# Performance work log

Measured on AMD Instinct MI355X. Metric: run time of the kernel, lower is better.

Reference implementation:

```python
import jax, jax.numpy as jnp
import numpy as np

E, H, D = 400000, 8, 64  # edges, num_head, dim_dh
N, G = 40000, 10000      # nodes, generated nodes
PRO = 30000              # pro_nodes_num


def setup_inputs() -> dict:
    key = jax.random.key(0)
    ks = jax.random.split(key, 12)
    a_ij = jax.random.normal(ks[0], (E, H, D), dtype=jnp.float32)
    pos = jax.random.normal(ks[1], (N, 3), dtype=jnp.float32)
    generate_node_dist = jax.random.uniform(ks[2], (G,), dtype=jnp.float32)
    edge_index = jax.random.randint(ks[3], (2, E), 0, N, dtype=jnp.int64)
    parent_node_idxes = jax.random.randint(ks[4], (G,), 0, N, dtype=jnp.int64)
    generate_node_idxes = jax.random.randint(ks[5], (G,), 0, N, dtype=jnp.int64)
    mask_edge_inv = jax.random.randint(ks[6], (E, 1), 0, 2, dtype=jnp.int32).astype(jnp.bool_)
    # MLP params: Linear(D, D//2) -> LeakyReLU -> Linear(D//2, 1); head mixer Linear(H, 1, bias=False)
    W1 = jax.random.normal(ks[7], (D, D // 2), dtype=jnp.float32) / np.sqrt(D)
    b1 = jnp.zeros((D // 2,), dtype=jnp.float32)
    W2 = jax.random.normal(ks[8], (D // 2,), dtype=jnp.float32) / np.sqrt(D // 2)
    b2 = jnp.zeros((1,), dtype=jnp.float32)
    Wh = jax.random.normal(ks[9], (H,), dtype=jnp.float32) / np.sqrt(H)
    return {
        "a_ij": a_ij, "pos": pos, "generate_node_dist": generate_node_dist,
        "edge_index": edge_index, "parent_node_idxes": parent_node_idxes,
        "generate_node_idxes": generate_node_idxes, "mask_edge_inv": mask_edge_inv,
        "pro_nodes_num": PRO,
        "W1": W1, "b1": b1, "W2": W2, "b2": b2, "Wh": Wh,
    }


def reference(a_ij, pos, generate_node_dist, edge_index, parent_node_idxes,
              generate_node_idxes, mask_edge_inv, pro_nodes_num,
              W1, b1, W2, b2, Wh):
    src, dst = edge_index[0], edge_index[1]  # [E]
    # Original filters edges where src >= pro_nodes_num; we keep static shapes and
    # zero the contribution of filtered edges instead (identical scatter-sum result).
    edge_keep = src >= pro_nodes_num                       # [E]
    valid = edge_keep & (~mask_edge_inv[:, 0])             # [E]

    delta_x = pos[src] - pos[dst]                          # [E,3]
    norm = jnp.linalg.norm(delta_x, axis=-1, keepdims=True)
    delta_x = delta_x / (norm + 1e-6)
    delta_x = jnp.where(valid[:, None], delta_x, 0.0)      # mask_edge_inv + dropped edges

    # attention2deltax MLP (dropout inactive at inference): [E,H,D] -> [E,H]
    h = jax.nn.leaky_relu(jnp.einsum('ehd,df->ehf', a_ij, W1) + b1)
    s = jnp.einsum('ehf,f->eh', h, W2) + b2                # [E,H]
    attention = jnp.einsum('eh,h->e', s, Wh)               # weighted_head_layer, [E]

    delta_x = delta_x * attention[:, None]                 # [E,3]
    agg = jax.ops.segment_sum(delta_x, src, num_segments=pos.shape[0])  # [N,3]
    return pos[generate_node_idxes] + agg[generate_node_idxes]
```

## Files before the change

kernel.cpp:

```cpp
#include <hip/hip_runtime.h>

typedef short s8v __attribute__((ext_vector_type(8)));
typedef float f4v __attribute__((ext_vector_type(4)));
typedef unsigned short u16;
typedef unsigned int   u32;
typedef unsigned long long u64;

#define NHEAD 8
#define FDIM  32

__device__ __forceinline__ u16 f2bf(float f) {
    u32 u = __float_as_uint(f);
    u32 r = u + 0x7fffu + ((u >> 16) & 1u);
    return (u16)(r >> 16);
}

__device__ __forceinline__ void detect_ints(const void* maskp, const void* eidxp,
                                            int lane, int& mbyte, int& i64f) {
    u32 mkw = ((const u32*)maskp)[lane];
    mbyte = (__ballot(mkw > 1u) != 0ull) ? 1 : 0;
    u32 od = ((const u32*)eidxp)[2 * lane + 1];
    i64f = (__ballot(od != 0u) == 0ull) ? 1 : 0;
}

struct WaveCtx {
    s8v bfrag[2][2];
    float sumWh, b2v, b1c0, b1c1, w2c0, w2c1;
    float wh0, wh1, wh2, wh3;
};

__device__ __forceinline__ WaveCtx setup_wave(int lane,
    const void* W1p, const void* b1p, const void* W2p, const void* b2p, const void* Whp)
{
    WaveCtx w;
    const int c0 = lane & 15;
    const int krow = (lane >> 4) * 8;
    const int hi4  = (lane >> 4) & 1;
    const float* w1 = (const float*)W1p; const float* b1 = (const float*)b1p;
    const float* w2 = (const float*)W2p; const float* b2 = (const float*)b2p;
    const float* wh = (const float*)Whp;
    float WhV[NHEAD]; w.sumWh = 0.f;
    #pragma unroll
    for (int h = 0; h < NHEAD; ++h) { WhV[h] = wh[h]; w.sumWh += WhV[h]; }
    w.b2v = b2[0];
    w.b1c0 = b1[c0]; w.b1c1 = b1[c0 + 16];
    w.w2c0 = w2[c0]; w.w2c1 = w2[c0 + 16];
    #pragma unroll
    for (int cb = 0; cb < 2; ++cb)
        #pragma unroll
        for (int kh = 0; kh < 2; ++kh)
            #pragma unroll
            for (int j = 0; j < 8; ++j) {
                int k = kh * 32 + krow + j;
                w.bfrag[cb][kh][j] = (short)f2bf(w1[k * FDIM + cb * 16 + c0]);
            }
    w.wh0 = hi4 ? WhV[4] : WhV[0];
    w.wh1 = hi4 ? WhV[5] : WhV[1];
    w.wh2 = hi4 ? WhV[6] : WhV[2];
    w.wh3 = hi4 ? WhV[7] : WhV[3];
    return w;
}

__device__ __forceinline__ void load_tile(const float* a32, int edge, int row, int krow,
                                          s8v& a0, s8v& a1)
{
    const size_t rowbase = ((size_t)edge * 8 + (size_t)(row & 7)) * 64 + (size_t)krow;
    const f4v* p = (const f4v*)(a32 + rowbase);
    f4v v0 = p[0], v1 = p[1], v2 = p[8], v3 = p[9];
    #pragma unroll
    for (int j = 0; j < 4; ++j) {
        a0[j]     = (short)f2bf(v0[j]);
        a0[j + 4] = (short)f2bf(v1[j]);
        a1[j]     = (short)f2bf(v2[j]);
        a1[j + 4] = (short)f2bf(v3[j]);
    }
}

__device__ __forceinline__ float tile_att(const WaveCtx& w, const s8v& a0, const s8v& a1)
{
    f4v C0 = {0.f,0.f,0.f,0.f}, C1 = {0.f,0.f,0.f,0.f};
    C0 = __builtin_amdgcn_mfma_f32_16x16x32_bf16(a0, w.bfrag[0][0], C0, 0, 0, 0);
    C0 = __builtin_amdgcn_mfma_f32_16x16x32_bf16(a1, w.bfrag[0][1], C0, 0, 0, 0);
    C1 = __builtin_amdgcn_mfma_f32_16x16x32_bf16(a0, w.bfrag[1][0], C1, 0, 0, 0);
    C1 = __builtin_amdgcn_mfma_f32_16x16x32_bf16(a1, w.bfrag[1][1], C1, 0, 0, 0);

    float partial;
    {
        float x0, x1, trow;
        x0 = C0[0] + w.b1c0; x0 = (x0 >= 0.f) ? x0 : 0.01f * x0;
        x1 = C1[0] + w.b1c1; x1 = (x1 >= 0.f) ? x1 : 0.01f * x1;
        trow = x0 * w.w2c0 + x1 * w.w2c1; partial  = trow * w.wh0;
        x0 = C0[1] + w.b1c0; x0 = (x0 >= 0.f) ? x0 : 0.01f * x0;
        x1 = C1[1] + w.b1c1; x1 = (x1 >= 0.f) ? x1 : 0.01f * x1;
        trow = x0 * w.w2c0 + x1 * w.w2c1; partial += trow * w.wh1;
        x0 = C0[2] + w.b1c0; x0 = (x0 >= 0.f) ? x0 : 0.01f * x0;
        x1 = C1[2] + w.b1c1; x1 = (x1 >= 0.f) ? x1 : 0.01f * x1;
        trow = x0 * w.w2c0 + x1 * w.w2c1; partial += trow * w.wh2;
        x0 = C0[3] + w.b1c0; x0 = (x0 >= 0.f) ? x0 : 0.01f * x0;
        x1 = C1[3] + w.b1c1; x1 = (x1 >= 0.f) ? x1 : 0.01f * x1;
        trow = x0 * w.w2c0 + x1 * w.w2c1; partial += trow * w.wh3;
    }
    partial += __shfl_xor(partial, 1);
    partial += __shfl_xor(partial, 2);
    partial += __shfl_xor(partial, 4);
    partial += __shfl_xor(partial, 8);
    partial += __shfl_xor(partial, 16);
    return partial + w.b2v * w.sumWh;
}

__global__ __launch_bounds__(256)
void zero_kernel(float* __restrict__ agg, u32* __restrict__ ind, int N3, int N)
{
    int i = blockIdx.x * blockDim.x + threadIdx.x;
    if (i < N3) agg[i] = 0.f;
    if (i < N)  ind[i] = 0u;
}

__global__ __launch_bounds__(256)
void mark_kernel(const void* __restrict__ gidxp, u32* __restrict__ ind,
                 const void* __restrict__ maskp, const void* __restrict__ eidxp, int G)
{
    const int lane = threadIdx.x & 63;
    int mbyte, i64f;
    detect_ints(maskp, eidxp, lane, mbyte, i64f);
    (void)mbyte;
    int g = blockIdx.x * blockDim.x + threadIdx.x;
    if (g >= G) return;
    const int idx = i64f ? (int)((const long long*)gidxp)[g] : ((const int*)gidxp)[g];
    ind[idx] = 1u;
}

__global__ __launch_bounds__(256, 4)
void attn_kernel(const void* __restrict__ a_ij,
                 const void* __restrict__ pos,
                 const void* __restrict__ eidx,
                 const void* __restrict__ maskp,
                 const int*  __restrict__ proP,
                 const void* __restrict__ W1p,
                 const void* __restrict__ b1p,
                 const void* __restrict__ W2p,
                 const void* __restrict__ b2p,
                 const void* __restrict__ Whp,
                 float* __restrict__ agg,
                 const u32* __restrict__ ind,
                 int E)
{
    __shared__ float attbuf[4][68];
    __shared__ int   idxbuf[4][68];

    const int lane = threadIdx.x & 63;
    const int wv   = threadIdx.x >> 6;
    const int gw = blockIdx.x * 4 + wv;
    const int nchunks = (E + 63) >> 6;
    if (gw >= nchunks) return;

    const int base = gw << 6;
    const int ie = base + lane;

    const int*   e32 = (const int*)eidx;
    const long long* e64 = (const long long*)eidx;
    const unsigned char* m8 = (const unsigned char*)maskp;
    const int*   m32 = (const int*)maskp;

    int s32 = 0; long long s64 = 0; int m8v = 1;
    if (ie < E) { s32 = e32[ie]; s64 = e64[ie]; m8v = (int)m8[ie]; }
    const int pro = proP[0];

    int mbyte, i64f;
    detect_ints(maskp, eidx, lane, mbyte, i64f);

    const int srcv = i64f ? (int)s64 : s32;
    int mk = 1;
    if (ie < E) mk = mbyte ? m8v : m32[ie];

    const u32 need = ind[srcv];

    const WaveCtx w = setup_wave(lane, W1p, b1p, W2p, b2p, Whp);

    const bool v = (ie < E) && (srcv >= pro) && (mk == 0) && (need != 0u);
    const u64 msav = __ballot(v);
    const int nv = __popcll(msav);
    if (nv == 0) return;

    const int off = __popcll(msav & ((1ull << lane) - 1ull));
    if (v) idxbuf[wv][off] = lane;
    asm volatile("s_waitcnt lgkmcnt(0)" ::: "memory");

    const int bp = idxbuf[wv][(lane < nv) ? lane : 0] & 63;
    const int s  = __shfl(srcv, bp);

    float px = 0.f, py = 0.f, pz = 0.f, qx = 0.f, qy = 0.f, qz = 0.f;
    if (lane < nv) {
        const int e = base + bp;
        const int d = i64f ? (int)e64[E + e] : e32[E + e];
        const float* pp = (const float*)pos;
        px = pp[3 * s]; py = pp[3 * s + 1]; pz = pp[3 * s + 2];
        qx = pp[3 * d]; qy = pp[3 * d + 1]; qz = pp[3 * d + 2];
    }

    const float* a32 = (const float*)a_ij;
    const int krow = (lane >> 4) * 8;
    const int row  = lane & 15;

    u64 m0 = msav;
    auto pop = [&](int& dst) -> bool {
        if (m0) { dst = __builtin_ctzll(m0); m0 &= m0 - 1; return true; }
        return false;
    };

    int slot = 0;
    while (m0) {
        int ba, bb, bc, bd;
        pop(ba);
        bool h1 = pop(bb); if (!h1) bb = ba;
        bool h2 = pop(bc);
        bool h3 = false;
        if (h2) { h3 = pop(bd); if (!h3) bd = bc; }

        s8v x0, x1, y0, y1;
        load_tile(a32, base + ((row < 8) ? ba : bb), row, krow, x0, x1);
        if (h2) load_tile(a32, base + ((row < 8) ? bc : bd), row, krow, y0, y1);

        const float atA = tile_att(w, x0, x1);
        if ((lane & 31) == 0) attbuf[wv][slot + (lane >> 5)] = atA;
        int adv = 1 + (h1 ? 1 : 0);
        if (h2) {
            const float atB = tile_att(w, y0, y1);
            if ((lane & 31) == 0) attbuf[wv][slot + adv + (lane >> 5)] = atB;
            adv += 1 + (h3 ? 1 : 0);
        }
        slot += adv;
    }

    asm volatile("s_waitcnt lgkmcnt(0)" ::: "memory");

    if (lane < nv) {
        const float att = attbuf[wv][lane];
        const float dx = px - qx, dy = py - qy, dz = pz - qz;
        const float nrm = sqrtf(dx * dx + dy * dy + dz * dz) + 1e-6f;
        const float sc = att / nrm;
        atomicAdd(&agg[3 * s + 0], dx * sc);
        atomicAdd(&agg[3 * s + 1], dy * sc);
        atomicAdd(&agg[3 * s + 2], dz * sc);
    }
}

__global__ __launch_bounds__(256)
void finalize_kernel(const void* __restrict__ pos,
                     const void* __restrict__ gidxp,
                     const float* __restrict__ agg,
                     float* __restrict__ outp,
                     const void* __restrict__ maskp,
                     const void* __restrict__ eidxp,
                     int G)
{
    const int lane = threadIdx.x & 63;
    int mbyte, i64f;
    detect_ints(maskp, eidxp, lane, mbyte, i64f);
    (void)mbyte;

    int g = blockIdx.x * blockDim.x + threadIdx.x;
    if (g >= G) return;
    const int idx = i64f ? (int)((const long long*)gidxp)[g] : ((const int*)gidxp)[g];
    const float* pp = (const float*)pos;
    #pragma unroll
    for (int c = 0; c < 3; ++c) {
        outp[3 * g + c] = pp[3 * idx + c] + agg[3 * idx + c];
    }
}

extern "C" void kernel_launch(void* const* d_in, const int* in_sizes, int n_in,
                              void* d_out, int out_size, void* d_ws, size_t ws_size,
                              hipStream_t stream) {
    const void* a_ij = d_in[0];
    const void* pos  = d_in[1];
    const void* eidx = d_in[3];
    const void* gidx = d_in[5];
    const void* mask = d_in[6];
    const int*  pro  = (const int*)d_in[7];
    const void* W1   = d_in[8];
    const void* b1   = d_in[9];
    const void* W2   = d_in[10];
    const void* b2   = d_in[11];
    const void* Wh   = d_in[12];

    const int E  = in_sizes[3] / 2;
    const int N  = in_sizes[1] / 3;
    const int N3 = N * 3;
    const int G  = in_sizes[5];

    float* agg = (float*)d_ws;
    u32*   ind = (u32*)((char*)d_ws + (((size_t)N3 * 4 + 255) & ~(size_t)255));

    zero_kernel<<<(N3 + 255) / 256, 256, 0, stream>>>(agg, ind, N3, N);

    mark_kernel<<<(G + 255) / 256, 256, 0, stream>>>(gidx, ind, mask, eidx, G);

    const int nchunks = (E + 63) >> 6;
    const int nblocks = (nchunks + 3) / 4;
    attn_kernel<<<nblocks, 256, 0, stream>>>(a_ij, pos, eidx, mask, pro,
                                             W1, b1, W2, b2, Wh, agg, ind, E);

    finalize_kernel<<<(G + 255) / 256, 256, 0, stream>>>(pos, gidx, agg, (float*)d_out,
                                                         mask, eidx, G);
}
```

Before: 27.06 us.

## Compact valid edges into a global list before dense attention MLP

Splits the fused attention kernel into a scan kernel, which compacts the edges that survive filtering into global index/src/dst lists using a wave ballot and an atomic counter, and a persistent dense kernel that processes 8 compacted edges per wave iteration. Because only about a tenth of edges survive, the old per-64-edge waves ran sparse, imbalanced MLP loops; compaction is meant to give every wave full tiles of work. The cost is an extra kernel launch, global list writes and reads, and loss of ordering locality in the a_ij gathers.

```diff
diff --git a/kernel.cpp b/kernel.cpp
--- a/kernel.cpp
+++ b/kernel.cpp
@@ -109,11 +109,13 @@
 }
 
 __global__ __launch_bounds__(256)
-void zero_kernel(float* __restrict__ agg, u32* __restrict__ ind, int N3, int N)
+void init_kernel(float* __restrict__ agg, u32* __restrict__ ind, int* __restrict__ cnt,
+                 int N3, int N)
 {
     int i = blockIdx.x * blockDim.x + threadIdx.x;
     if (i < N3) agg[i] = 0.f;
     if (i < N)  ind[i] = 0u;
+    if (i == 0) cnt[0] = 0;
 }
 
 __global__ __launch_bounds__(256)
@@ -130,27 +132,19 @@
     ind[idx] = 1u;
 }
 
-__global__ __launch_bounds__(256, 4)
-void attn_kernel(const void* __restrict__ a_ij,
-                 const void* __restrict__ pos,
-                 const void* __restrict__ eidx,
+__global__ __launch_bounds__(256)
+void scan_kernel(const void* __restrict__ eidx,
                  const void* __restrict__ maskp,
                  const int*  __restrict__ proP,
-                 const void* __restrict__ W1p,
-                 const void* __restrict__ b1p,
-                 const void* __restrict__ W2p,
-                 const void* __restrict__ b2p,
-                 const void* __restrict__ Whp,
-                 float* __restrict__ agg,
                  const u32* __restrict__ ind,
+                 int* __restrict__ cnt,
+                 int* __restrict__ list,
+                 int* __restrict__ srcl,
+                 int* __restrict__ dstl,
                  int E)
 {
-    __shared__ float attbuf[4][68];
-    __shared__ int   idxbuf[4][68];
-
     const int lane = threadIdx.x & 63;
-    const int wv   = threadIdx.x >> 6;
-    const int gw = blockIdx.x * 4 + wv;
+    const int gw = blockIdx.x * 4 + (threadIdx.x >> 6);
     const int nchunks = (E + 63) >> 6;
     if (gw >= nchunks) return;
 
@@ -172,76 +166,103 @@
     const int srcv = i64f ? (int)s64 : s32;
     int mk = 1;
     if (ie < E) mk = mbyte ? m8v : m32[ie];
-
     const u32 need = ind[srcv];
 
+    const bool v = (ie < E) && (srcv >= pro) && (mk == 0) && (need != 0u);
+    const u64 bal = __ballot(v);
+    const int nv = __popcll(bal);
+    if (nv == 0) return;
+
+    int basei = 0;
+    if (lane == 0) basei = atomicAdd(cnt, nv);
+    basei = __shfl(basei, 0);
+
+    if (v) {
+        const int off = __popcll(bal & ((1ull << lane) - 1ull));
+        const int d = i64f ? (int)e64[E + ie] : e32[E + ie];
+        list[basei + off] = ie;
+        srcl[basei + off] = srcv;
+        dstl[basei + off] = d;
+    }
+}
+
+__global__ __launch_bounds__(256, 4)
+void dense_kernel(const void* __restrict__ a_ij,
+                  const void* __restrict__ pos,
+                  const void* __restrict__ W1p,
+                  const void* __restrict__ b1p,
+                  const void* __restrict__ W2p,
+                  const void* __restrict__ b2p,
+                  const void* __restrict__ Whp,
+                  float* __restrict__ agg,
+                  const int* __restrict__ cnt,
+                  const int* __restrict__ list,
+                  const int* __restrict__ srcl,
+                  const int* __restrict__ dstl)
+{
+    const int lane = threadIdx.x & 63;
+    const int gwave = blockIdx.x * 4 + (threadIdx.x >> 6);
+    const int nw = gridDim.x * 4;
+
+    const int count = cnt[0];
+    if (gwave * 8 >= count) return;
+
     const WaveCtx w = setup_wave(lane, W1p, b1p, W2p, b2p, Whp);
 
-    const bool v = (ie < E) && (srcv >= pro) && (mk == 0) && (need != 0u);
-    const u64 msav = __ballot(v);
-    const int nv = __popcll(msav);
-    if (nv == 0) return;
-
-    const int off = __popcll(msav & ((1ull << lane) - 1ull));
-    if (v) idxbuf[wv][off] = lane;
-    asm volatile("s_waitcnt lgkmcnt(0)" ::: "memory");
-
-    const int bp = idxbuf[wv][(lane < nv) ? lane : 0] & 63;
-    const int s  = __shfl(srcv, bp);
-
-    float px = 0.f, py = 0.f, pz = 0.f, qx = 0.f, qy = 0.f, qz = 0.f;
-    if (lane < nv) {
-        const int e = base + bp;
-        const int d = i64f ? (int)e64[E + e] : e32[E + e];
-        const float* pp = (const float*)pos;
-        px = pp[3 * s]; py = pp[3 * s + 1]; pz = pp[3 * s + 2];
-        qx = pp[3 * d]; qy = pp[3 * d + 1]; qz = pp[3 * d + 2];
-    }
-
     const float* a32 = (const float*)a_ij;
+    const float* pp  = (const float*)pos;
     const int krow = (lane >> 4) * 8;
     const int row  = lane & 15;
-
-    u64 m0 = msav;
-    auto pop = [&](int& dst) -> bool {
-        if (m0) { dst = __builtin_ctzll(m0); m0 &= m0 - 1; return true; }
-        return false;
-    };
-
-    int slot = 0;
-    while (m0) {
-        int ba, bb, bc, bd;
-        pop(ba);
-        bool h1 = pop(bb); if (!h1) bb = ba;
-        bool h2 = pop(bc);
-        bool h3 = false;
-        if (h2) { h3 = pop(bd); if (!h3) bd = bc; }
-
-        s8v x0, x1, y0, y1;
-        load_tile(a32, base + ((row < 8) ? ba : bb), row, krow, x0, x1);
-        if (h2) load_tile(a32, base + ((row < 8) ? bc : bd), row, krow, y0, y1);
-
-        const float atA = tile_att(w, x0, x1);
-        if ((lane & 31) == 0) attbuf[wv][slot + (lane >> 5)] = atA;
-        int adv = 1 + (h1 ? 1 : 0);
-        if (h2) {
-            const float atB = tile_att(w, y0, y1);
-            if ((lane & 31) == 0) attbuf[wv][slot + adv + (lane >> 5)] = atB;
-            adv += 1 + (h3 ? 1 : 0);
+    const int rsel = (row < 8) ? 0 : 1;
+
+    for (int t = gwave; t * 8 < count; t += nw) {
+        const int base8 = t * 8;
+        const int np = min(8, count - base8);
+        int slot = base8 + (lane & 7);
+        if (slot > count - 1) slot = count - 1;
+
+        const int eid  = list[slot];
+        const int esrc = srcl[slot];
+        const int edst = dstl[slot];
+
+        float px = 0.f, py = 0.f, pz = 0.f, qx = 0.f, qy = 0.f, qz = 0.f;
+        if (lane < np) {
+            px = pp[3 * esrc]; py = pp[3 * esrc + 1]; pz = pp[3 * esrc + 2];
+            qx = pp[3 * edst]; qy = pp[3 * edst + 1]; qz = pp[3 * edst + 2];
         }
-        slot += adv;
-    }
-
-    asm volatile("s_waitcnt lgkmcnt(0)" ::: "memory");
-
-    if (lane < nv) {
-        const float att = attbuf[wv][lane];
-        const float dx = px - qx, dy = py - qy, dz = pz - qz;
-        const float nrm = sqrtf(dx * dx + dy * dy + dz * dz) + 1e-6f;
-        const float sc = att / nrm;
-        atomicAdd(&agg[3 * s + 0], dx * sc);
-        atomicAdd(&agg[3 * s + 1], dy * sc);
-        atomicAdd(&agg[3 * s + 2], dz * sc);
+
+        const int e0 = __shfl(eid, 0 + rsel);
+        const int e1 = __shfl(eid, 2 + rsel);
+        const int e2 = __shfl(eid, 4 + rsel);
+        const int e3 = __shfl(eid, 6 + rsel);
+
+        s8v x0, x1, y0, y1, z0, z1, u0, u1;
+        load_tile(a32, e0, row, krow, x0, x1);
+        load_tile(a32, e1, row, krow, y0, y1);
+        load_tile(a32, e2, row, krow, z0, z1);
+        load_tile(a32, e3, row, krow, u0, u1);
+
+        const float at0 = tile_att(w, x0, x1);
+        const float at1 = tile_att(w, y0, y1);
+        const float at2 = tile_att(w, z0, z1);
+        const float at3 = tile_att(w, u0, u1);
+        const float at0o = __shfl(at0, 32);
+        const float at1o = __shfl(at1, 32);
+        const float at2o = __shfl(at2, 32);
+        const float at3o = __shfl(at3, 32);
+
+        if (lane < np) {
+            const int k = lane >> 1;
+            const float ate = (k == 0) ? at0 : (k == 1) ? at1 : (k == 2) ? at2 : at3;
+            const float ato = (k == 0) ? at0o : (k == 1) ? at1o : (k == 2) ? at2o : at3o;
+            const float att = (lane & 1) ? ato : ate;
+            const float dx = px - qx, dy = py - qy, dz = pz - qz;
+            const float nrm = sqrtf(dx * dx + dy * dy + dz * dz) + 1e-6f;
+            const float sc = att / nrm;
+            atomicAdd(&agg[3 * esrc + 0], dx * sc);
+            atomicAdd(&agg[3 * esrc + 1], dy * sc);
+            atomicAdd(&agg[3 * esrc + 2], dz * sc);
+        }
     }
 }
 
@@ -289,17 +310,24 @@
     const int N3 = N * 3;
     const int G  = in_sizes[5];
 
-    float* agg = (float*)d_ws;
-    u32*   ind = (u32*)((char*)d_ws + (((size_t)N3 * 4 + 255) & ~(size_t)255));
-
-    zero_kernel<<<(N3 + 255) / 256, 256, 0, stream>>>(agg, ind, N3, N);
+    char* p = (char*)d_ws;
+    float* agg = (float*)p;                 p += ((size_t)N3 * 4 + 255) & ~(size_t)255;
+    u32*   ind = (u32*)p;                   p += ((size_t)N  * 4 + 255) & ~(size_t)255;
+    int*   cnt = (int*)p;                   p += 256;
+    int*   list = (int*)p;                  p += ((size_t)E * 4 + 255) & ~(size_t)255;
+    int*   srcl = (int*)p;                  p += ((size_t)E * 4 + 255) & ~(size_t)255;
+    int*   dstl = (int*)p;
+
+    init_kernel<<<(N3 + 255) / 256, 256, 0, stream>>>(agg, ind, cnt, N3, N);
 
     mark_kernel<<<(G + 255) / 256, 256, 0, stream>>>(gidx, ind, mask, eidx, G);
 
     const int nchunks = (E + 63) >> 6;
-    const int nblocks = (nchunks + 3) / 4;
-    attn_kernel<<<nblocks, 256, 0, stream>>>(a_ij, pos, eidx, mask, pro,
-                                             W1, b1, W2, b2, Wh, agg, ind, E);
+    scan_kernel<<<(nchunks + 3) / 4, 256, 0, stream>>>(eidx, mask, pro, ind, cnt,
+                                                       list, srcl, dstl, E);
+
+    dense_kernel<<<512, 256, 0, stream>>>(a_ij, pos, W1, b1, W2, b2, Wh,
+                                          agg, cnt, list, srcl, dstl);
 
     finalize_kernel<<<(G + 255) / 256, 256, 0, stream>>>(pos, gidx, agg, (float*)d_out,
                                                          mask, eidx, G);
```

After: 86.16 us. 218% more time.
